# Performance work log

Hardware: AMD Instinct MI355X
Metric: run time of the kernel (lower is better)

Reference implementation:

```python
import jax, jax.numpy as jnp
import numpy as np

N_NODES = 50000
HIDDEN = 128
N_REL = 9
N_LAYERS = 3
N_EDGES = 600000


def setup_inputs() -> dict:
    key = jax.random.key(0)
    k1, k2, k3, k4, k5 = jax.random.split(key, 5)
    edge_index = jax.random.randint(k1, (2, N_EDGES), 0, N_NODES, dtype=jnp.int64 if jax.config.jax_enable_x64 else jnp.int32)
    edge_type = jax.random.randint(k2, (N_EDGES,), 0, N_REL, dtype=edge_index.dtype)
    embeddings = jax.random.uniform(k3, (N_NODES, HIDDEN), dtype=jnp.float32)
    weights = jax.random.uniform(k4, (N_LAYERS, N_REL, HIDDEN, HIDDEN), dtype=jnp.float32)
    biases = jax.random.uniform(k5, (N_LAYERS, N_REL, HIDDEN), dtype=jnp.float32)
    return {"edge_index": edge_index, "edge_type": edge_type,
            "embeddings": embeddings, "weights": weights, "biases": biases}


def reference(edge_index, edge_type, embeddings, weights, biases):
    # RGCN: per relation r, messages = emb[src] @ W[l,r] + b[l,r], scatter-summed
    # into dest. Equivalent vectorized form: precompute X = emb @ W for all
    # relations ([R,N,E]), then a single gather + segment_sum over edges.
    L = weights.shape[0]
    N = embeddings.shape[0]
    dest = edge_index[0]
    src = edge_index[1]
    out = embeddings
    for l in range(L):
        X = jnp.einsum('ne,ref->rnf', out, weights[l])        # [R, N, E]
        msg = X[edge_type, src] + biases[l][edge_type]        # [num_edges, E]
        hidden = jax.ops.segment_sum(msg, dest, num_segments=N)  # [N, E]
        if l + 1 < L:
            hidden = jax.nn.relu(hidden)
        out = hidden
    return out
```

## Files before the change

### kernel.cpp

```cpp
#include <hip/hip_runtime.h>

#define NNODES 50000
#define HID 128
#define NREL 9
#define NLAYERS 3
#define NEDGES 600000

#define NBINS (NREL * NNODES)
#define SCAN_CHUNK 1024
#define NBLK ((NBINS + SCAN_CHUNK - 1) / SCAN_CHUNK)

#define KTOT (NREL * HID)
#define GM2 128
#define BK 64
#define PITCH 72
#define EPITCH 136

typedef __attribute__((ext_vector_type(8))) short short8;
typedef __attribute__((ext_vector_type(4))) float f32x4;

__device__ __forceinline__ short f2bf(float f) {
    union { float f; unsigned u; } c; c.f = f;
    unsigned r = c.u + 0x7fff + ((c.u >> 16) & 1);
    return (short)(r >> 16);
}
__device__ __forceinline__ float bf2f(short v) {
    return __uint_as_float(((unsigned)(unsigned short)v) << 16);
}


__global__ void hist2_kernel(const int* __restrict__ dst, const int* __restrict__ etype,
                             int* __restrict__ bins) {
    int e = blockIdx.x * blockDim.x + threadIdx.x;
    if (e < NEDGES) {
        int bin = dst[e] * NREL + etype[e];
        atomicAdd(&bins[bin], 1);
    }
}

__global__ __launch_bounds__(256) void scan_pass1(const int* __restrict__ bins,
                                                  int* __restrict__ blocksum) {
    __shared__ int red[256];
    int b = blockIdx.x, t = threadIdx.x;
    int i0 = b * SCAN_CHUNK + t * 4;
    int s = 0;
#pragma unroll
    for (int k = 0; k < 4; k++)
        if (i0 + k < NBINS) s += bins[i0 + k];
    red[t] = s;
    __syncthreads();
    for (int off = 128; off > 0; off >>= 1) {
        if (t < off) red[t] += red[t + off];
        __syncthreads();
    }
    if (t == 0) blocksum[b] = red[0];
}

__global__ __launch_bounds__(512) void scan_pass2(const int* __restrict__ blocksum,
                                                  int* __restrict__ blockoff,
                                                  int* __restrict__ rowptr) {
    __shared__ int s[512];
    int t = threadIdx.x;
    int v = (t < NBLK) ? blocksum[t] : 0;
    s[t] = v;
    __syncthreads();
    for (int off = 1; off < 512; off <<= 1) {
        int x = (t >= off) ? s[t - off] : 0;
        __syncthreads();
        s[t] += x;
        __syncthreads();
    }
    if (t < NBLK) blockoff[t] = s[t] - v;
    if (t == 0) rowptr[NBINS] = NEDGES;
}

__global__ __launch_bounds__(256) void scan_pass3(const int* __restrict__ bins,
                                                  const int* __restrict__ blockoff,
                                                  int* __restrict__ rowptr,
                                                  int* __restrict__ cursor) {
    __shared__ int sc[256];
    int b = blockIdx.x, t = threadIdx.x;
    int i0 = b * SCAN_CHUNK + t * 4;
    int v[4], p[4];
    int s = 0;
#pragma unroll
    for (int k = 0; k < 4; k++) {
        v[k] = (i0 + k < NBINS) ? bins[i0 + k] : 0;
        p[k] = s;
        s += v[k];
    }
    sc[t] = s;
    __syncthreads();
    for (int off = 1; off < 256; off <<= 1) {
        int x = (t >= off) ? sc[t - off] : 0;
        __syncthreads();
        sc[t] += x;
        __syncthreads();
    }
    int base = blockoff[b] + (sc[t] - s);
#pragma unroll
    for (int k = 0; k < 4; k++) {
        if (i0 + k < NBINS) {
            rowptr[i0 + k] = base + p[k];
            cursor[i0 + k] = base + p[k];
        }
    }
}

__global__ void place_kernel(const int* __restrict__ dst, const int* __restrict__ src,
                             const int* __restrict__ etype,
                             int* __restrict__ cursor, int* __restrict__ bsrc) {
    int e = blockIdx.x * blockDim.x + threadIdx.x;
    if (e < NEDGES) {
        int bin = dst[e] * NREL + etype[e];
        int pos = atomicAdd(&cursor[bin], 1);
        bsrc[pos] = src[e];
    }
}


__global__ __launch_bounds__(256) void convert_w(const float* __restrict__ W,
                                                 short* __restrict__ Wt2) {
    int lr = blockIdx.x;
    int l = lr / NREL, r = lr - l * NREL;
    const float* w = W + (size_t)lr * HID * HID;
    short* o = Wt2 + (size_t)l * HID * KTOT;
    int tid = threadIdx.x;
#pragma unroll 4
    for (int i = 0; i < 64; i++) {
        int elem = i * 256 + tid;
        int kk = elem >> 7, n = elem & 127;
        o[(size_t)n * KTOT + r * HID + kk] = f2bf(w[elem]);
    }
}

__global__ __launch_bounds__(256) void convert_emb(const float* __restrict__ E,
                                                   short* __restrict__ Ebf) {
    int gid = blockIdx.x * blockDim.x + threadIdx.x;
    const float* p = E + (size_t)gid * 8;
    float4 v0 = *(const float4*)p;
    float4 v1 = *(const float4*)(p + 4);
    short8 o = {f2bf(v0.x), f2bf(v0.y), f2bf(v0.z), f2bf(v0.w),
                f2bf(v1.x), f2bf(v1.y), f2bf(v1.z), f2bf(v1.w)};
    *(short8*)(Ebf + (size_t)gid * 8) = o;
}


__global__ __launch_bounds__(256) void gather_kernel(const short* __restrict__ Hbf,
                                                     const int* __restrict__ bsrc,
                                                     const int* __restrict__ rowptr,
                                                     short* __restrict__ S) {
    int gid = blockIdx.x * blockDim.x + threadIdx.x;
    int bin = gid >> 3;
    if (bin >= NBINS) return;
    int ck  = gid & 7;
    int rs = rowptr[bin];
    int re = rowptr[bin + 1];
    float a[16];
#pragma unroll
    for (int i = 0; i < 16; i++) a[i] = 0.f;
    for (int j = rs; j < re; j++) {
        int s = bsrc[j];
        const short* hp = Hbf + (size_t)s * HID + ck * 16;
        short8 v0 = *(const short8*)hp;
        short8 v1 = *(const short8*)(hp + 8);
#pragma unroll
        for (int i = 0; i < 8; i++) a[i]     += bf2f(v0[i]);
#pragma unroll
        for (int i = 0; i < 8; i++) a[i + 8] += bf2f(v1[i]);
    }
    short8 o0 = {f2bf(a[0]),  f2bf(a[1]),  f2bf(a[2]),  f2bf(a[3]),
                 f2bf(a[4]),  f2bf(a[5]),  f2bf(a[6]),  f2bf(a[7])};
    short8 o1 = {f2bf(a[8]),  f2bf(a[9]),  f2bf(a[10]), f2bf(a[11]),
                 f2bf(a[12]), f2bf(a[13]), f2bf(a[14]), f2bf(a[15])};
    short* sp = S + (size_t)bin * HID + ck * 16;
    *(short8*)sp       = o0;
    *(short8*)(sp + 8) = o1;
}


__global__ __launch_bounds__(256) void gemm_kernel(const short* __restrict__ S,
                                                   const short* __restrict__ Wt2l,
                                                   const float* __restrict__ Bias,
                                                   const int* __restrict__ rowptr,
                                                   short* __restrict__ HoutBf,
                                                   float* __restrict__ HoutF,
                                                   int last) {
    __shared__ short lds[2 * GM2 * PITCH];
    __shared__ int   rp_s[GM2 * NREL + 1];
    __shared__ float bias_s[NREL * HID];
    short* As = lds;
    short* Bs = lds + GM2 * PITCH;

    int tid  = threadIdx.x;
    int wave = tid >> 6, lane = tid & 63;
    int row0 = blockIdx.x * GM2;
    int m0   = wave * 32;
    int lm = lane & 15, lq = lane >> 4;

    int rpbase = row0 * NREL;
    for (int i = tid; i <= GM2 * NREL; i += 256) {
        int g = rpbase + i;
        rp_s[i] = rowptr[(g < NBINS) ? g : NBINS];
    }
    for (int i = tid; i < NREL * HID; i += 256) bias_s[i] = Bias[i];

    f32x4 acc[2][8];
#pragma unroll
    for (int mf = 0; mf < 2; mf++)
#pragma unroll
        for (int nt = 0; nt < 8; nt++) acc[mf][nt] = (f32x4){0.f, 0.f, 0.f, 0.f};

    for (int kc = 0; kc < KTOT / BK; kc++) {
        __syncthreads();
#pragma unroll
        for (int i = 0; i < 4; i++) {
            int p = i * 256 + tid;
            int row = p >> 3, ck = p & 7;
            short8 va = *(const short8*)(S + (size_t)(row0 + row) * KTOT + kc * BK + ck * 8);
            *(short8*)&As[row * PITCH + ck * 8] = va;
            short8 vb = *(const short8*)(Wt2l + (size_t)row * KTOT + kc * BK + ck * 8);
            *(short8*)&Bs[row * PITCH + ck * 8] = vb;
        }
        __syncthreads();
#pragma unroll
        for (int ks = 0; ks < 2; ks++) {
            short8 af0 = *(const short8*)&As[(m0 + lm) * PITCH + ks * 32 + lq * 8];
            short8 af1 = *(const short8*)&As[(m0 + 16 + lm) * PITCH + ks * 32 + lq * 8];
#pragma unroll
            for (int nt = 0; nt < 8; nt++) {
                short8 bf = *(const short8*)&Bs[(nt * 16 + lm) * PITCH + ks * 32 + lq * 8];
                acc[0][nt] = __builtin_amdgcn_mfma_f32_16x16x32_bf16(af0, bf, acc[0][nt], 0, 0, 0);
                acc[1][nt] = __builtin_amdgcn_mfma_f32_16x16x32_bf16(af1, bf, acc[1][nt], 0, 0, 0);
            }
        }
    }
    __syncthreads();

    if (!last) {
        short (*Et)[EPITCH] = (short(*)[EPITCH])lds;
#pragma unroll
        for (int mf = 0; mf < 2; mf++) {
#pragma unroll
            for (int reg = 0; reg < 4; reg++) {
                int rl = m0 + mf * 16 + lq * 4 + reg;
                float cr[NREL];
#pragma unroll
                for (int r = 0; r < NREL; r++)
                    cr[r] = (float)(rp_s[rl * NREL + r + 1] - rp_s[rl * NREL + r]);
#pragma unroll
                for (int nt = 0; nt < 8; nt++) {
                    int n = nt * 16 + lm;
                    float b = 0.f;
#pragma unroll
                    for (int r = 0; r < NREL; r++) b += cr[r] * bias_s[r * HID + n];
                    float o = fmaxf(acc[mf][nt][reg] + b, 0.f);
                    Et[rl][n] = f2bf(o);
                }
            }
        }
        __syncthreads();
#pragma unroll
        for (int i = 0; i < 8; i++) {
            int p = i * 256 + tid;
            int row = p >> 4, ck = p & 15;
            int d = row0 + row;
            if (d < NNODES)
                *(short8*)(HoutBf + (size_t)d * HID + ck * 8) = *(const short8*)&Et[row][ck * 8];
        }
    } else {
#pragma unroll
        for (int mf = 0; mf < 2; mf++) {
#pragma unroll
            for (int reg = 0; reg < 4; reg++) {
                int rl = m0 + mf * 16 + lq * 4 + reg;
                int d  = row0 + rl;
                if (d >= NNODES) continue;
                float cr[NREL];
#pragma unroll
                for (int r = 0; r < NREL; r++)
                    cr[r] = (float)(rp_s[rl * NREL + r + 1] - rp_s[rl * NREL + r]);
#pragma unroll
                for (int nt = 0; nt < 8; nt++) {
                    int n = nt * 16 + lm;
                    float b = 0.f;
#pragma unroll
                    for (int r = 0; r < NREL; r++) b += cr[r] * bias_s[r * HID + n];
                    HoutF[(size_t)d * HID + n] = acc[mf][nt][reg] + b;
                }
            }
        }
    }
}


extern "C" void kernel_launch(void* const* d_in, const int* in_sizes, int n_in,
                              void* d_out, int out_size, void* d_ws, size_t ws_size,
                              hipStream_t stream) {
    const int*   edge_index = (const int*)d_in[0];
    const int*   etype      = (const int*)d_in[1];
    const float* emb        = (const float*)d_in[2];
    const float* W          = (const float*)d_in[3];
    const float* Bias       = (const float*)d_in[4];
    float*       out        = (float*)d_out;

    const int* dst  = edge_index;
    const int* srcA = edge_index + NEDGES;

    short* Ebf = (short*)d_ws;
    short* Hbf = Ebf + (size_t)NNODES * HID;
    short* S   = Hbf + (size_t)NNODES * HID;
    short* Wt2 = S + (size_t)NNODES * KTOT;
    int*   bsrc     = (int*)(Wt2 + (size_t)NLAYERS * HID * KTOT);
    int*   bins     = bsrc + NEDGES;
    int*   cursor   = bins + NBINS;
    int*   rowptr   = cursor + NBINS;
    int*   blocksum = rowptr + NBINS + 1;
    int*   blockoff = blocksum + NBLK;

    hipMemsetAsync(bins, 0, NBINS * sizeof(int), stream);
    hist2_kernel<<<(NEDGES + 255) / 256, 256, 0, stream>>>(dst, etype, bins);
    scan_pass1<<<NBLK, 256, 0, stream>>>(bins, blocksum);
    scan_pass2<<<1, 512, 0, stream>>>(blocksum, blockoff, rowptr);
    scan_pass3<<<NBLK, 256, 0, stream>>>(bins, blockoff, rowptr, cursor);
    place_kernel<<<(NEDGES + 255) / 256, 256, 0, stream>>>(dst, srcA, etype, cursor, bsrc);
    convert_w<<<NLAYERS * NREL, 256, 0, stream>>>(W, Wt2);
    convert_emb<<<(NNODES * HID / 8) / 256, 256, 0, stream>>>(emb, Ebf);

    const short* Hin = Ebf;
    for (int l = 0; l < NLAYERS; l++) {
        gather_kernel<<<(NBINS * 8 + 255) / 256, 256, 0, stream>>>(Hin, bsrc, rowptr, S);
        const short* Wtl = Wt2 + (size_t)l * HID * KTOT;
        const float* Bl  = Bias + (size_t)l * NREL * HID;
        int last = (l + 1 == NLAYERS);
        gemm_kernel<<<(NNODES + GM2 - 1) / GM2, 256, 0, stream>>>(
            S, Wtl, Bl, rowptr, Hbf, out, last);
        Hin = Hbf;
    }
}
```

Before: 515.1 us.

## Halve GEMM row tile and register-prefetch next K chunk

```diff
diff --git a/kernel.cpp b/kernel.cpp
--- a/kernel.cpp
+++ b/kernel.cpp
@@ -11,8 +11,9 @@
 #define NBLK ((NBINS + SCAN_CHUNK - 1) / SCAN_CHUNK)
 
 #define KTOT (NREL * HID)
-#define GM2 128
+#define GM2 64
 #define BK 64
+#define NCHUNK (KTOT / BK)
 #define PITCH 72
 #define EPITCH 136
 
@@ -186,7 +187,7 @@
                                                    short* __restrict__ HoutBf,
                                                    float* __restrict__ HoutF,
                                                    int last) {
-    __shared__ short lds[2 * GM2 * PITCH];
+    __shared__ short lds[GM2 * PITCH + HID * PITCH];
     __shared__ int   rp_s[GM2 * NREL + 1];
     __shared__ float bias_s[NREL * HID];
     short* As = lds;
@@ -195,7 +196,7 @@
     int tid  = threadIdx.x;
     int wave = tid >> 6, lane = tid & 63;
     int row0 = blockIdx.x * GM2;
-    int m0   = wave * 32;
+    int m0   = wave * 16;
     int lm = lane & 15, lq = lane >> 4;
 
     int rpbase = row0 * NREL;
@@ -205,89 +206,103 @@
     }
     for (int i = tid; i < NREL * HID; i += 256) bias_s[i] = Bias[i];
 
-    f32x4 acc[2][8];
-#pragma unroll
-    for (int mf = 0; mf < 2; mf++)
-#pragma unroll
-        for (int nt = 0; nt < 8; nt++) acc[mf][nt] = (f32x4){0.f, 0.f, 0.f, 0.f};
-
-    for (int kc = 0; kc < KTOT / BK; kc++) {
+    int rowL = tid >> 3;
+    int ck   = tid & 7;
+    int ar0 = row0 + rowL;        if (ar0 > NNODES - 1) ar0 = NNODES - 1;
+    int ar1 = row0 + 32 + rowL;   if (ar1 > NNODES - 1) ar1 = NNODES - 1;
+    const short* pA0 = S + (size_t)ar0 * KTOT + ck * 8;
+    const short* pA1 = S + (size_t)ar1 * KTOT + ck * 8;
+    const short* pB0 = Wt2l + (size_t)(rowL      ) * KTOT + ck * 8;
+    const short* pB1 = Wt2l + (size_t)(rowL + 32 ) * KTOT + ck * 8;
+    const short* pB2 = Wt2l + (size_t)(rowL + 64 ) * KTOT + ck * 8;
+    const short* pB3 = Wt2l + (size_t)(rowL + 96 ) * KTOT + ck * 8;
+
+    short8 ra0 = *(const short8*)pA0;
+    short8 ra1 = *(const short8*)pA1;
+    short8 rb0 = *(const short8*)pB0;
+    short8 rb1 = *(const short8*)pB1;
+    short8 rb2 = *(const short8*)pB2;
+    short8 rb3 = *(const short8*)pB3;
+
+    f32x4 acc[8];
+#pragma unroll
+    for (int nt = 0; nt < 8; nt++) acc[nt] = (f32x4){0.f, 0.f, 0.f, 0.f};
+
+    for (int kc = 0; kc < NCHUNK; kc++) {
+        __syncthreads();
+        *(short8*)&As[ rowL       * PITCH + ck * 8] = ra0;
+        *(short8*)&As[(rowL + 32) * PITCH + ck * 8] = ra1;
+        *(short8*)&Bs[ rowL       * PITCH + ck * 8] = rb0;
+        *(short8*)&Bs[(rowL + 32) * PITCH + ck * 8] = rb1;
+        *(short8*)&Bs[(rowL + 64) * PITCH + ck * 8] = rb2;
+        *(short8*)&Bs[(rowL + 96) * PITCH + ck * 8] = rb3;
+        __syncthreads();
+        if (kc + 1 < NCHUNK) {
+            int off = (kc + 1) * BK;
+            ra0 = *(const short8*)(pA0 + off);
+            ra1 = *(const short8*)(pA1 + off);
+            rb0 = *(const short8*)(pB0 + off);
+            rb1 = *(const short8*)(pB1 + off);
+            rb2 = *(const short8*)(pB2 + off);
+            rb3 = *(const short8*)(pB3 + off);
+        }
+#pragma unroll
+        for (int ks = 0; ks < 2; ks++) {
+            short8 af = *(const short8*)&As[(m0 + lm) * PITCH + ks * 32 + lq * 8];
+#pragma unroll
+            for (int nt = 0; nt < 8; nt++) {
+                short8 bf = *(const short8*)&Bs[(nt * 16 + lm) * PITCH + ks * 32 + lq * 8];
+                acc[nt] = __builtin_amdgcn_mfma_f32_16x16x32_bf16(af, bf, acc[nt], 0, 0, 0);
+            }
+        }
+    }
+    __syncthreads();
+
+    if (!last) {
+        short (*Et)[EPITCH] = (short(*)[EPITCH])lds;
+#pragma unroll
+        for (int reg = 0; reg < 4; reg++) {
+            int rl = m0 + lq * 4 + reg;
+            float cr[NREL];
+#pragma unroll
+            for (int r = 0; r < NREL; r++)
+                cr[r] = (float)(rp_s[rl * NREL + r + 1] - rp_s[rl * NREL + r]);
+#pragma unroll
+            for (int nt = 0; nt < 8; nt++) {
+                int n = nt * 16 + lm;
+                float b = 0.f;
+#pragma unroll
+                for (int r = 0; r < NREL; r++) b += cr[r] * bias_s[r * HID + n];
+                float o = fmaxf(acc[nt][reg] + b, 0.f);
+                Et[rl][n] = f2bf(o);
+            }
+        }
         __syncthreads();
 #pragma unroll
         for (int i = 0; i < 4; i++) {
             int p = i * 256 + tid;
-            int row = p >> 3, ck = p & 7;
-            short8 va = *(const short8*)(S + (size_t)(row0 + row) * KTOT + kc * BK + ck * 8);
-            *(short8*)&As[row * PITCH + ck * 8] = va;
-            short8 vb = *(const short8*)(Wt2l + (size_t)row * KTOT + kc * BK + ck * 8);
-            *(short8*)&Bs[row * PITCH + ck * 8] = vb;
-        }
-        __syncthreads();
-#pragma unroll
-        for (int ks = 0; ks < 2; ks++) {
-            short8 af0 = *(const short8*)&As[(m0 + lm) * PITCH + ks * 32 + lq * 8];
-            short8 af1 = *(const short8*)&As[(m0 + 16 + lm) * PITCH + ks * 32 + lq * 8];
-#pragma unroll
-            for (int nt = 0; nt < 8; nt++) {
-                short8 bf = *(const short8*)&Bs[(nt * 16 + lm) * PITCH + ks * 32 + lq * 8];
-                acc[0][nt] = __builtin_amdgcn_mfma_f32_16x16x32_bf16(af0, bf, acc[0][nt], 0, 0, 0);
-                acc[1][nt] = __builtin_amdgcn_mfma_f32_16x16x32_bf16(af1, bf, acc[1][nt], 0, 0, 0);
-            }
-        }
-    }
-    __syncthreads();
-
-    if (!last) {
-        short (*Et)[EPITCH] = (short(*)[EPITCH])lds;
-#pragma unroll
-        for (int mf = 0; mf < 2; mf++) {
-#pragma unroll
-            for (int reg = 0; reg < 4; reg++) {
-                int rl = m0 + mf * 16 + lq * 4 + reg;
-                float cr[NREL];
-#pragma unroll
-                for (int r = 0; r < NREL; r++)
-                    cr[r] = (float)(rp_s[rl * NREL + r + 1] - rp_s[rl * NREL + r]);
-#pragma unroll
-                for (int nt = 0; nt < 8; nt++) {
-                    int n = nt * 16 + lm;
-                    float b = 0.f;
-#pragma unroll
-                    for (int r = 0; r < NREL; r++) b += cr[r] * bias_s[r * HID + n];
-                    float o = fmaxf(acc[mf][nt][reg] + b, 0.f);
-                    Et[rl][n] = f2bf(o);
-                }
-            }
-        }
-        __syncthreads();
-#pragma unroll
-        for (int i = 0; i < 8; i++) {
-            int p = i * 256 + tid;
-            int row = p >> 4, ck = p & 15;
+            int row = p >> 4, cc = p & 15;
             int d = row0 + row;
             if (d < NNODES)
-                *(short8*)(HoutBf + (size_t)d * HID + ck * 8) = *(const short8*)&Et[row][ck * 8];
+                *(short8*)(HoutBf + (size_t)d * HID + cc * 8) = *(const short8*)&Et[row][cc * 8];
         }
     } else {
 #pragma unroll
-        for (int mf = 0; mf < 2; mf++) {
-#pragma unroll
-            for (int reg = 0; reg < 4; reg++) {
-                int rl = m0 + mf * 16 + lq * 4 + reg;
-                int d  = row0 + rl;
-                if (d >= NNODES) continue;
-                float cr[NREL];
-#pragma unroll
-                for (int r = 0; r < NREL; r++)
-                    cr[r] = (float)(rp_s[rl * NREL + r + 1] - rp_s[rl * NREL + r]);
-#pragma unroll
-                for (int nt = 0; nt < 8; nt++) {
-                    int n = nt * 16 + lm;
-                    float b = 0.f;
-#pragma unroll
-                    for (int r = 0; r < NREL; r++) b += cr[r] * bias_s[r * HID + n];
-                    HoutF[(size_t)d * HID + n] = acc[mf][nt][reg] + b;
-                }
+        for (int reg = 0; reg < 4; reg++) {
+            int rl = m0 + lq * 4 + reg;
+            int d  = row0 + rl;
+            if (d >= NNODES) continue;
+            float cr[NREL];
+#pragma unroll
+            for (int r = 0; r < NREL; r++)
+                cr[r] = (float)(rp_s[rl * NREL + r + 1] - rp_s[rl * NREL + r]);
+#pragma unroll
+            for (int nt = 0; nt < 8; nt++) {
+                int n = nt * 16 + lm;
+                float b = 0.f;
+#pragma unroll
+                for (int r = 0; r < NREL; r++) b += cr[r] * bias_s[r * HID + n];
+                HoutF[(size_t)d * HID + n] = acc[nt][reg] + b;
             }
         }
     }
```

Result: faster. 441.2 us (-14.4%).
